# Optimization experiments

Hardware: AMD Instinct MI355X
Metric: run time of the kernel (lower is better)

The kernel has to match this reference:

```python
import jax, jax.numpy as jnp
import numpy as np

CAPS = 16          # num_capsules
DIM = 16           # capsule_dim
NUM_ROUTING = 3
L2_EPS = 1e-12     # tf.nn.l2_normalize epsilon


def setup_inputs() -> dict:
    key = jax.random.key(0)
    k1, k2 = jax.random.split(key)
    inputs = jax.random.normal(k1, (16, 64, 64, 128), dtype=jnp.float32)
    # Conv2D kernel, HWIO layout, fan-in scaled like glorot-ish init
    kernel = jax.random.normal(k2, (3, 3, 128, CAPS * DIM), dtype=jnp.float32) * 0.03
    bias = jnp.zeros((CAPS * DIM,), dtype=jnp.float32)
    return {"inputs": inputs, "kernel": kernel, "bias": bias}


def reference(inputs, kernel, bias):
    # Conv2D(caps*dim, 3x3, padding='same', activation='relu'), channels_last
    x = jax.lax.conv_general_dilated(
        inputs, kernel, window_strides=(1, 1), padding="SAME",
        dimension_numbers=("NHWC", "HWIO", "NHWC"))
    x = jax.nn.relu(x + bias)
    B, H, W, _ = x.shape
    x = x.reshape(B, H * W, CAPS, DIM)            # (B, N, C, D)
    b = jnp.zeros((B, H * W, CAPS), dtype=x.dtype)
    v = None
    for _ in range(NUM_ROUTING):
        c = jax.nn.softmax(b, axis=-1)             # over capsules
        s = jnp.einsum("bnc,bncd->bcd", c, x)      # weighted sum over spatial
        # tf.nn.l2_normalize along last axis
        v = s * jax.lax.rsqrt(jnp.maximum(jnp.sum(s * s, axis=-1, keepdims=True), L2_EPS))
        b = b + jnp.einsum("bncd,bcd->bnc", x, v)  # agreement update
    # tile v over spatial dims: (B,1,1,C*D) -> (B,H,W,C*D)
    out = jnp.broadcast_to(v.reshape(B, 1, 1, CAPS * DIM), (B, H, W, CAPS * DIM))
    return out
```

## Files before the change

kernel.cpp:

```cpp
#include <hip/hip_runtime.h>
#include <hip/hip_bf16.h>

typedef unsigned short u16;
typedef unsigned int   u32;

typedef __bf16 bf16x8 __attribute__((ext_vector_type(8)));
typedef float  f32x4  __attribute__((ext_vector_type(4)));

#define GLDS(gp, lp) __builtin_amdgcn_global_load_lds( \
    (const __attribute__((address_space(1))) void*)(gp), \
    (__attribute__((address_space(3))) void*)(lp), 16, 0, 0)

__device__ __forceinline__ u16 f2b(float f) {
    __hip_bfloat16 h = __float2bfloat16(f);
    u16 u; __builtin_memcpy(&u, &h, 2); return u;
}
__device__ __forceinline__ float blo(u32 u) { return __uint_as_float(u << 16); }
__device__ __forceinline__ float bhi(u32 u) { return __uint_as_float(u & 0xffff0000u); }

__global__ void k_prep(const float* __restrict__ in, const float* __restrict__ wk,
                       u16* __restrict__ pad, u16* __restrict__ BF,
                       float* __restrict__ stats) {
    int bx = blockIdx.x, tid = threadIdx.x;
    if (bx < 4356) {
        int idx = bx * 256 + tid;
        int e0  = idx * 8;
        int ch  = e0 & 127;
        int rest = e0 >> 7;
        int pw = rest % 66;
        int r2 = rest / 66;
        int ph = r2 % 66;
        int b  = r2 / 66;
        u16 ov[8];
        if (ph >= 1 && ph <= 64 && pw >= 1 && pw <= 64) {
            const float* src = in + (((b * 64 + (ph - 1)) * 64 + (pw - 1)) * 128 + ch);
            const float4* s4 = (const float4*)src;
            float4 f0 = s4[0], f1 = s4[1];
            ov[0]=f2b(f0.x); ov[1]=f2b(f0.y); ov[2]=f2b(f0.z); ov[3]=f2b(f0.w);
            ov[4]=f2b(f1.x); ov[5]=f2b(f1.y); ov[6]=f2b(f1.z); ov[7]=f2b(f1.w);
        } else {
            #pragma unroll
            for (int j = 0; j < 8; ++j) ov[j] = 0;
        }
        uint4 w; __builtin_memcpy(&w, ov, 16);
        *(uint4*)(pad + e0) = w;
    } else if (bx < 5508) {
        int t = (bx - 4356) * 256 + tid;
        int j  = t & 7;
        int n  = (t >> 3) & 255;
        int q  = (t >> 11) & 3;
        int kk = (t >> 13) & 3;
        int p  = t >> 15;
        BF[t] = f2b(wk[(p * 128 + kk * 32 + q * 8 + j) * 256 + n]);
    } else {
        stats[(bx - 5508) * 256 + tid] = 0.f;
    }
}

__launch_bounds__(256, 2)
__global__ void k_conv(const u16* __restrict__ Ap, const u16* __restrict__ BF,
                       const float* __restrict__ bias,
                       u16* __restrict__ X, float* __restrict__ s0) {
    __shared__ u16 ldsA[12672];
    const int t = threadIdx.x;
    const int lane = t & 63, wid = t >> 6;
    const int q = lane >> 4, l15 = lane & 15;
    const int bb = blockIdx.x >> 6;
    const int h  = blockIdx.x & 63;
    const int wn0 = wid << 6;

#define STAGE(S) { \
    const int sb0 = wid * 396; \
    _Pragma("unroll") for (int i = 0; i < 6; ++i) { \
        int sb = sb0 + i * 64; \
        int slot = sb + lane; \
        int pr = slot / 528; int rem = slot - pr * 528; \
        int wp = rem >> 3, cs = rem & 7; \
        int gc = (S) * 8 + (cs ^ (wp & 7)); \
        const u16* g = Ap + ((((bb * 66 + h + pr) * 66 + wp) << 7) + (gc << 3)); \
        GLDS(g, (char*)ldsA + sb * 16); \
    } \
    { int sb = sb0 + 384; \
      if (lane < 12) { \
        int slot = sb + lane; \
        int pr = slot / 528; int rem = slot - pr * 528; \
        int wp = rem >> 3, cs = rem & 7; \
        int gc = (S) * 8 + (cs ^ (wp & 7)); \
        const u16* g = Ap + ((((bb * 66 + h + pr) * 66 + wp) << 7) + (gc << 3)); \
        GLDS(g, (char*)ldsA + sb * 16); \
      } } }

#define LOADB(B, P, S) { \
    _Pragma("unroll") for (int kk = 0; kk < 2; ++kk) \
    _Pragma("unroll") for (int ni = 0; ni < 4; ++ni) \
        B[kk * 4 + ni] = *(const bf16x8*)(BFl + (P) * 32768 + \
                                          ((S) * 2 + kk) * 8192 + ni * 128); }

#define COMPP(B, DH, DW) { \
    _Pragma("unroll") for (int kk = 0; kk < 2; ++kk) { \
        bf16x8 af[4]; \
        _Pragma("unroll") for (int mi = 0; mi < 4; ++mi) { \
            int wp = mi * 16 + l15 + (DW); \
            int swz = (kk * 4 + q) ^ (wp & 7); \
            af[mi] = *(const bf16x8*)((const char*)ldsA + \
                (((DH) * 528 + wp * 8 + swz) << 4)); \
        } \
        _Pragma("unroll") for (int mi = 0; mi < 4; ++mi) \
        _Pragma("unroll") for (int ni = 0; ni < 4; ++ni) \
            acc[mi][ni] = __builtin_amdgcn_mfma_f32_16x16x32_bf16( \
                af[mi], B[kk * 4 + ni], acc[mi][ni], 0, 0, 0); } }

    const u16* BFl = BF + (q * 2048 + (wn0 + l15) * 8);

    f32x4 zero = {0.f, 0.f, 0.f, 0.f};
    f32x4 acc[4][4];
    #pragma unroll
    for (int mi = 0; mi < 4; ++mi)
        #pragma unroll
        for (int ni = 0; ni < 4; ++ni) acc[mi][ni] = zero;

    bf16x8 B0[8], B1[8];

    STAGE(0);
    __syncthreads();
    LOADB(B0, 0, 0);
    LOADB(B1, 1, 0); COMPP(B0, 0, 0);
    LOADB(B0, 2, 0); COMPP(B1, 0, 1);
    LOADB(B1, 3, 0); COMPP(B0, 0, 2);
    LOADB(B0, 4, 0); COMPP(B1, 1, 0);
    LOADB(B1, 5, 0); COMPP(B0, 1, 1);
    LOADB(B0, 6, 0); COMPP(B1, 1, 2);
    LOADB(B1, 7, 0); COMPP(B0, 2, 0);
    LOADB(B0, 8, 0); COMPP(B1, 2, 1);
    COMPP(B0, 2, 2);
    __syncthreads();

    STAGE(1);
    __syncthreads();
    LOADB(B0, 0, 1);
    LOADB(B1, 1, 1); COMPP(B0, 0, 0);
    LOADB(B0, 2, 1); COMPP(B1, 0, 1);
    LOADB(B1, 3, 1); COMPP(B0, 0, 2);
    LOADB(B0, 4, 1); COMPP(B1, 1, 0);
    LOADB(B1, 5, 1); COMPP(B0, 1, 1);
    LOADB(B0, 6, 1); COMPP(B1, 1, 2);
    LOADB(B1, 7, 1); COMPP(B0, 2, 0);
    LOADB(B0, 8, 1); COMPP(B1, 2, 1);
    COMPP(B0, 2, 2);

    float bv[4];
    #pragma unroll
    for (int ni = 0; ni < 4; ++ni) bv[ni] = bias[wn0 + ni * 16 + l15];
    float colsum[4] = {0.f, 0.f, 0.f, 0.f};
    u16* xrow = X + (((bb << 12) + (h << 6) + q * 4) * 256) + wn0 + l15;
    #pragma unroll
    for (int mi = 0; mi < 4; ++mi) {
        #pragma unroll
        for (int rr = 0; rr < 4; ++rr) {
            u16* xp = xrow + (mi * 16 + rr) * 256;
            #pragma unroll
            for (int ni = 0; ni < 4; ++ni) {
                float v = acc[mi][ni][rr] + bv[ni];
                v = v > 0.f ? v : 0.f;
                xp[ni * 16] = f2b(v);
                colsum[ni] += v;
            }
        }
    }
    #pragma unroll
    for (int ni = 0; ni < 4; ++ni) {
        float c = colsum[ni];
        c += __shfl_xor(c, 16);
        c += __shfl_xor(c, 32);
        if (lane < 16) atomicAdd(&s0[bb * 256 + wn0 + ni * 16 + l15], c);
    }
#undef STAGE
#undef LOADB
#undef COMPP
}

__launch_bounds__(256, 4)
__global__ void k_pass(const u16* __restrict__ X, const float* __restrict__ Sa,
                       const float* __restrict__ Sb, float* __restrict__ Sout,
                       int use2) {
    __shared__ float v1s[272], v2s[272];
    __shared__ float red[4 * 272];
    const int t = threadIdx.x, b = blockIdx.y, chunk = blockIdx.x;
    const int c = t & 15, nl = t >> 4;
    const int lane = t & 63, wid = t >> 6;
    {
        float sa = Sa[b * 256 + t];
        float ss = sa * sa;
        #pragma unroll
        for (int off = 1; off < 16; off <<= 1) ss += __shfl_xor(ss, off);
        ss = ss < 1e-12f ? 1e-12f : ss;
        v1s[(t >> 4) * 17 + (t & 15)] = sa / sqrtf(ss);
        if (use2) {
            float sb = Sb[b * 256 + t];
            float s2v = sb * sb;
            #pragma unroll
            for (int off = 1; off < 16; off <<= 1) s2v += __shfl_xor(s2v, off);
            s2v = s2v < 1e-12f ? 1e-12f : s2v;
            v2s[(t >> 4) * 17 + (t & 15)] = sb / sqrtf(s2v);
        } else {
            v2s[(t >> 4) * 17 + (t & 15)] = 0.f;
        }
    }
    const u16* xbase = X + ((b << 12) + chunk * 64 + nl) * 256 + c * 16;
    uint4 pa[8];
    #pragma unroll
    for (int r = 0; r < 4; ++r) {
        pa[2 * r]     = ((const uint4*)(xbase + r * 16 * 256))[0];
        pa[2 * r + 1] = ((const uint4*)(xbase + r * 16 * 256))[1];
    }
    __syncthreads();
    float v1r[16], v2r[16];
    #pragma unroll
    for (int d = 0; d < 16; ++d) { v1r[d] = v1s[c * 17 + d]; v2r[d] = v2s[c * 17 + d]; }

    float acc[16];
    #pragma unroll
    for (int d = 0; d < 16; ++d) acc[d] = 0.f;

    #pragma unroll
    for (int r = 0; r < 4; ++r) {
        u32 us[8];
        __builtin_memcpy(us, &pa[2 * r], 32);
        float xf[16];
        #pragma unroll
        for (int j = 0; j < 8; ++j) { xf[2*j] = blo(us[j]); xf[2*j+1] = bhi(us[j]); }
        float d1 = 0.f, d2 = 0.f;
        #pragma unroll
        for (int d = 0; d < 16; ++d) {
            d1 += xf[d] * v1r[d];
            d2 += xf[d] * v2r[d];
        }
        float bvv = use2 ? (d1 + d2) : d1;
        float e = __expf(bvv);
        float sm = e;
        #pragma unroll
        for (int off = 1; off < 16; off <<= 1) sm += __shfl_xor(sm, off);
        float w = e / sm;
        #pragma unroll
        for (int d = 0; d < 16; ++d) acc[d] += w * xf[d];
    }
    #pragma unroll
    for (int d = 0; d < 16; ++d) {
        acc[d] += __shfl_xor(acc[d], 16);
        acc[d] += __shfl_xor(acc[d], 32);
    }
    if (lane < 16) {
        #pragma unroll
        for (int d = 0; d < 16; ++d) red[wid * 272 + lane * 17 + d] = acc[d];
    }
    __syncthreads();
    {
        int c2 = t >> 4, d2 = t & 15;
        float tot = red[c2 * 17 + d2]       + red[272 + c2 * 17 + d2]
                  + red[544 + c2 * 17 + d2] + red[816 + c2 * 17 + d2];
        atomicAdd(&Sout[b * 256 + t], tot);
    }
}

__launch_bounds__(256, 4)
__global__ void k_bcast(const float* __restrict__ S, float* __restrict__ Out) {
    __shared__ float vls[256];
    int t = threadIdx.x, bx = blockIdx.x, b = blockIdx.y;
    float s = S[b * 256 + t];
    float ss = s * s;
    #pragma unroll
    for (int off = 1; off < 16; off <<= 1) ss += __shfl_xor(ss, off);
    ss = ss < 1e-12f ? 1e-12f : ss;
    vls[t] = s / sqrtf(ss);
    __syncthreads();
    float4 myv = ((const float4*)vls)[t & 63];
    float4* o = (float4*)Out + (long)b * 262144 + bx * 4096;
    #pragma unroll
    for (int j = 0; j < 16; ++j) o[j * 256 + t] = myv;
}

extern "C" void kernel_launch(void* const* d_in, const int* in_sizes, int n_in,
                              void* d_out, int out_size, void* d_ws, size_t ws_size,
                              hipStream_t stream) {
    const float* in   = (const float*)d_in[0];
    const float* wk   = (const float*)d_in[1];
    const float* bias = (const float*)d_in[2];
    float* out = (float*)d_out;
    char* ws = (char*)d_ws;

    const size_t OFF_PAD = 0;
    const size_t OFF_BF  = 17842176;
    const size_t OFF_X   = 18432000;
    const size_t OFF_ST  = 51986432;
    const size_t NEEDED  = OFF_ST + 3 * 16384;
    if (ws_size < NEEDED) return;

    u16* pad = (u16*)(ws + OFF_PAD);
    u16* BF  = (u16*)(ws + OFF_BF);
    u16* X   = (u16*)(ws + OFF_X);
    float* s0 = (float*)(ws + OFF_ST);
    float* s2 = s0 + 4096;
    float* s3 = s2 + 4096;

    k_prep <<<5556, 256, 0, stream>>>(in, wk, pad, BF, s0);
    k_conv <<<1024, 256, 0, stream>>>(pad, BF, bias, X, s0);
    k_pass <<<dim3(64, 16), 256, 0, stream>>>(X, s0, s0, s2, 0);
    k_pass <<<dim3(64, 16), 256, 0, stream>>>(X, s0, s2, s3, 1);
    k_bcast<<<dim3(64, 16), 256, 0, stream>>>(s3, out);
}
```

Measured before the change: 162.7 us.

## Fuse input padding and bf16 conversion into conv staging; enlarge routing pass chunks

Removes the separate padded bf16 copy of the input. The conv kernel now reads fp32 input directly, converts it and zero-fills borders while staging into LDS, replacing the async global-to-LDS loads. The routing pass merges its two v vectors into one summed vector, giving a single dot product. It also processes 256 positions per block with software-prefetched loads, using a quarter as many blocks. This saves one full write and read of the padded tensor, but conv staging becomes synchronous register loads, so latency hiding may suffer.

```diff
diff --git a/kernel.cpp b/kernel.cpp
--- a/kernel.cpp
+++ b/kernel.cpp
@@ -6,10 +6,6 @@
 
 typedef __bf16 bf16x8 __attribute__((ext_vector_type(8)));
 typedef float  f32x4  __attribute__((ext_vector_type(4)));
-
-#define GLDS(gp, lp) __builtin_amdgcn_global_load_lds( \
-    (const __attribute__((address_space(1))) void*)(gp), \
-    (__attribute__((address_space(3))) void*)(lp), 16, 0, 0)
 
 __device__ __forceinline__ u16 f2b(float f) {
     __hip_bfloat16 h = __float2bfloat16(f);
@@ -18,34 +14,11 @@
 __device__ __forceinline__ float blo(u32 u) { return __uint_as_float(u << 16); }
 __device__ __forceinline__ float bhi(u32 u) { return __uint_as_float(u & 0xffff0000u); }
 
-__global__ void k_prep(const float* __restrict__ in, const float* __restrict__ wk,
-                       u16* __restrict__ pad, u16* __restrict__ BF,
-                       float* __restrict__ stats) {
+__global__ void k_prep(const float* __restrict__ wk,
+                       u16* __restrict__ BF, float* __restrict__ stats) {
     int bx = blockIdx.x, tid = threadIdx.x;
-    if (bx < 4356) {
-        int idx = bx * 256 + tid;
-        int e0  = idx * 8;
-        int ch  = e0 & 127;
-        int rest = e0 >> 7;
-        int pw = rest % 66;
-        int r2 = rest / 66;
-        int ph = r2 % 66;
-        int b  = r2 / 66;
-        u16 ov[8];
-        if (ph >= 1 && ph <= 64 && pw >= 1 && pw <= 64) {
-            const float* src = in + (((b * 64 + (ph - 1)) * 64 + (pw - 1)) * 128 + ch);
-            const float4* s4 = (const float4*)src;
-            float4 f0 = s4[0], f1 = s4[1];
-            ov[0]=f2b(f0.x); ov[1]=f2b(f0.y); ov[2]=f2b(f0.z); ov[3]=f2b(f0.w);
-            ov[4]=f2b(f1.x); ov[5]=f2b(f1.y); ov[6]=f2b(f1.z); ov[7]=f2b(f1.w);
-        } else {
-            #pragma unroll
-            for (int j = 0; j < 8; ++j) ov[j] = 0;
-        }
-        uint4 w; __builtin_memcpy(&w, ov, 16);
-        *(uint4*)(pad + e0) = w;
-    } else if (bx < 5508) {
-        int t = (bx - 4356) * 256 + tid;
+    if (bx < 1152) {
+        int t = bx * 256 + tid;
         int j  = t & 7;
         int n  = (t >> 3) & 255;
         int q  = (t >> 11) & 3;
@@ -53,12 +26,12 @@
         int p  = t >> 15;
         BF[t] = f2b(wk[(p * 128 + kk * 32 + q * 8 + j) * 256 + n]);
     } else {
-        stats[(bx - 5508) * 256 + tid] = 0.f;
+        stats[(bx - 1152) * 256 + tid] = 0.f;
     }
 }
 
 __launch_bounds__(256, 2)
-__global__ void k_conv(const u16* __restrict__ Ap, const u16* __restrict__ BF,
+__global__ void k_conv(const float* __restrict__ in, const u16* __restrict__ BF,
                        const float* __restrict__ bias,
                        u16* __restrict__ X, float* __restrict__ s0) {
     __shared__ u16 ldsA[12672];
@@ -71,24 +44,27 @@
 
 #define STAGE(S) { \
     const int sb0 = wid * 396; \
-    _Pragma("unroll") for (int i = 0; i < 6; ++i) { \
-        int sb = sb0 + i * 64; \
-        int slot = sb + lane; \
-        int pr = slot / 528; int rem = slot - pr * 528; \
-        int wp = rem >> 3, cs = rem & 7; \
-        int gc = (S) * 8 + (cs ^ (wp & 7)); \
-        const u16* g = Ap + ((((bb * 66 + h + pr) * 66 + wp) << 7) + (gc << 3)); \
-        GLDS(g, (char*)ldsA + sb * 16); \
-    } \
-    { int sb = sb0 + 384; \
-      if (lane < 12) { \
-        int slot = sb + lane; \
-        int pr = slot / 528; int rem = slot - pr * 528; \
-        int wp = rem >> 3, cs = rem & 7; \
-        int gc = (S) * 8 + (cs ^ (wp & 7)); \
-        const u16* g = Ap + ((((bb * 66 + h + pr) * 66 + wp) << 7) + (gc << 3)); \
-        GLDS(g, (char*)ldsA + sb * 16); \
-      } } }
+    _Pragma("unroll") for (int i = 0; i < 7; ++i) { \
+        int slot = sb0 + i * 64 + lane; \
+        if (i < 6 || lane < 12) { \
+            int pr = slot / 528; int rem = slot - pr * 528; \
+            int wp = rem >> 3, cs = rem & 7; \
+            int gc = (S) * 8 + (cs ^ (wp & 7)); \
+            int y = h + pr - 1, x = wp - 1; \
+            u16 ov[8]; \
+            if (y >= 0 && y < 64 && x >= 0 && x < 64) { \
+                const float4* s4 = (const float4*)(in + \
+                    (((bb * 64 + y) * 64 + x) * 128 + gc * 8)); \
+                float4 f0 = s4[0], f1 = s4[1]; \
+                ov[0]=f2b(f0.x); ov[1]=f2b(f0.y); ov[2]=f2b(f0.z); ov[3]=f2b(f0.w); \
+                ov[4]=f2b(f1.x); ov[5]=f2b(f1.y); ov[6]=f2b(f1.z); ov[7]=f2b(f1.w); \
+            } else { \
+                _Pragma("unroll") for (int j = 0; j < 8; ++j) ov[j] = 0; \
+            } \
+            uint4 wv; __builtin_memcpy(&wv, ov, 16); \
+            *(uint4*)((char*)ldsA + slot * 16) = wv; \
+        } \
+    } }
 
 #define LOADB(B, P, S) { \
     _Pragma("unroll") for (int kk = 0; kk < 2; ++kk) \
@@ -183,59 +159,59 @@
 __global__ void k_pass(const u16* __restrict__ X, const float* __restrict__ Sa,
                        const float* __restrict__ Sb, float* __restrict__ Sout,
                        int use2) {
-    __shared__ float v1s[272], v2s[272];
+    __shared__ float vs[272];
     __shared__ float red[4 * 272];
     const int t = threadIdx.x, b = blockIdx.y, chunk = blockIdx.x;
     const int c = t & 15, nl = t >> 4;
     const int lane = t & 63, wid = t >> 6;
+    const u16* xbase = X + ((b << 12) + chunk * 256 + nl) * 256 + c * 16;
+
+    uint4 pa[4][2];
+    #pragma unroll
+    for (int r0 = 0; r0 < 4; ++r0) {
+        pa[r0][0] = ((const uint4*)(xbase + r0 * 4096))[0];
+        pa[r0][1] = ((const uint4*)(xbase + r0 * 4096))[1];
+    }
     {
         float sa = Sa[b * 256 + t];
         float ss = sa * sa;
         #pragma unroll
         for (int off = 1; off < 16; off <<= 1) ss += __shfl_xor(ss, off);
         ss = ss < 1e-12f ? 1e-12f : ss;
-        v1s[(t >> 4) * 17 + (t & 15)] = sa / sqrtf(ss);
+        float vv = sa / sqrtf(ss);
         if (use2) {
             float sb = Sb[b * 256 + t];
             float s2v = sb * sb;
             #pragma unroll
             for (int off = 1; off < 16; off <<= 1) s2v += __shfl_xor(s2v, off);
             s2v = s2v < 1e-12f ? 1e-12f : s2v;
-            v2s[(t >> 4) * 17 + (t & 15)] = sb / sqrtf(s2v);
-        } else {
-            v2s[(t >> 4) * 17 + (t & 15)] = 0.f;
+            vv += sb / sqrtf(s2v);
         }
-    }
-    const u16* xbase = X + ((b << 12) + chunk * 64 + nl) * 256 + c * 16;
-    uint4 pa[8];
-    #pragma unroll
-    for (int r = 0; r < 4; ++r) {
-        pa[2 * r]     = ((const uint4*)(xbase + r * 16 * 256))[0];
-        pa[2 * r + 1] = ((const uint4*)(xbase + r * 16 * 256))[1];
-    }
-    __syncthreads();
-    float v1r[16], v2r[16];
-    #pragma unroll
-    for (int d = 0; d < 16; ++d) { v1r[d] = v1s[c * 17 + d]; v2r[d] = v2s[c * 17 + d]; }
+        vs[(t >> 4) * 17 + (t & 15)] = vv;
+    }
+    __syncthreads();
+    float vr[16];
+    #pragma unroll
+    for (int d = 0; d < 16; ++d) vr[d] = vs[c * 17 + d];
 
     float acc[16];
     #pragma unroll
     for (int d = 0; d < 16; ++d) acc[d] = 0.f;
 
     #pragma unroll
-    for (int r = 0; r < 4; ++r) {
-        u32 us[8];
-        __builtin_memcpy(us, &pa[2 * r], 32);
+    for (int r = 0; r < 16; ++r) {
+        uint4 a0 = pa[r & 3][0], a1 = pa[r & 3][1];
+        if (r < 12) {
+            pa[r & 3][0] = ((const uint4*)(xbase + (r + 4) * 4096))[0];
+            pa[r & 3][1] = ((const uint4*)(xbase + (r + 4) * 4096))[1];
+        }
+        u32 us[8] = {a0.x, a0.y, a0.z, a0.w, a1.x, a1.y, a1.z, a1.w};
         float xf[16];
         #pragma unroll
         for (int j = 0; j < 8; ++j) { xf[2*j] = blo(us[j]); xf[2*j+1] = bhi(us[j]); }
-        float d1 = 0.f, d2 = 0.f;
-        #pragma unroll
-        for (int d = 0; d < 16; ++d) {
-            d1 += xf[d] * v1r[d];
-            d2 += xf[d] * v2r[d];
-        }
-        float bvv = use2 ? (d1 + d2) : d1;
+        float bvv = 0.f;
+        #pragma unroll
+        for (int d = 0; d < 16; ++d) bvv += xf[d] * vr[d];
         float e = __expf(bvv);
         float sm = e;
         #pragma unroll
@@ -288,23 +264,21 @@
     float* out = (float*)d_out;
     char* ws = (char*)d_ws;
 
-    const size_t OFF_PAD = 0;
-    const size_t OFF_BF  = 17842176;
-    const size_t OFF_X   = 18432000;
-    const size_t OFF_ST  = 51986432;
+    const size_t OFF_BF  = 0;
+    const size_t OFF_X   = 589824;
+    const size_t OFF_ST  = 34144256;
     const size_t NEEDED  = OFF_ST + 3 * 16384;
     if (ws_size < NEEDED) return;
 
-    u16* pad = (u16*)(ws + OFF_PAD);
     u16* BF  = (u16*)(ws + OFF_BF);
     u16* X   = (u16*)(ws + OFF_X);
     float* s0 = (float*)(ws + OFF_ST);
     float* s2 = s0 + 4096;
     float* s3 = s2 + 4096;
 
-    k_prep <<<5556, 256, 0, stream>>>(in, wk, pad, BF, s0);
-    k_conv <<<1024, 256, 0, stream>>>(pad, BF, bias, X, s0);
-    k_pass <<<dim3(64, 16), 256, 0, stream>>>(X, s0, s0, s2, 0);
-    k_pass <<<dim3(64, 16), 256, 0, stream>>>(X, s0, s2, s3, 1);
+    k_prep <<<1200, 256, 0, stream>>>(wk, BF, s0);
+    k_conv <<<1024, 256, 0, stream>>>(in, BF, bias, X, s0);
+    k_pass <<<dim3(16, 16), 256, 0, stream>>>(X, s0, s0, s2, 0);
+    k_pass <<<dim3(16, 16), 256, 0, stream>>>(X, s0, s2, s3, 1);
     k_bcast<<<dim3(64, 16), 256, 0, stream>>>(s3, out);
 }
```

New measurement: 191.7 us. 17.8% more time.
